# Optimization experiments

Hardware: AMD Instinct MI355X
Metric: run time of the kernel (lower is better)

The kernel has to match this reference:

```python
import jax, jax.numpy as jnp
import numpy as np

EPS = 1e-4
HEADS = 8
DIM_HEAD = 32
BALANCE = 0.3


def _normalize(x, dims):
    # torch normalize(): norm over `dims` in fp32; norm = eps + norm*sqrt(norm.numel()/x.numel())
    red = 1
    for d in dims:
        red *= x.shape[d]
    norm = jnp.sqrt(jnp.sum(jnp.square(x.astype(jnp.float32)), axis=dims, keepdims=True))
    norm = EPS + norm / np.sqrt(red)
    return x / norm.astype(x.dtype)


def _mpconv1x1(x, w, gain=1.0):
    # MPConv forward (eval mode): weight-normalize per output channel, scale, 1x1 conv
    w = w.astype(jnp.float32)
    w = _normalize(w, (1, 2, 3))
    fan_in = w.shape[1] * w.shape[2] * w.shape[3]
    w = (w * (gain / np.sqrt(fan_in))).astype(x.dtype)[:, :, 0, 0]  # [out, in]
    return jnp.einsum('oi,nihw->nohw', w, x)


def setup_inputs() -> dict:
    key = jax.random.key(0)
    k1, k2, k3 = jax.random.split(key, 3)
    x = jax.random.normal(k1, (2, 256, 48, 48), dtype=jnp.float32)
    w_qkv = jax.random.normal(k2, (768, 256, 1, 1), dtype=jnp.float32)
    w_out = jax.random.normal(k3, (256, 256, 1, 1), dtype=jnp.float32)
    return {"x": x, "w_qkv": w_qkv, "w_out": w_out}


def reference(x, w_qkv, w_out):
    n, c, h, w_sp = x.shape
    seq = h * w_sp
    y = _mpconv1x1(x, w_qkv)                          # [n, 3c, h, w]
    y = y.reshape(n, HEADS, DIM_HEAD, 3, seq)         # channel split: head x dim_head x 3
    y = _normalize(y, (2,))                           # L2-normalize over dim_head axis
    q = y[:, :, :, 0, :]
    k = y[:, :, :, 1, :]
    v = y[:, :, :, 2, :]
    # scores [n, h, q, k] with k scaled by 1/sqrt(dim_head)
    att = jax.nn.softmax(jnp.einsum('nhcq,nhck->nhqk', q, k) / np.sqrt(DIM_HEAD), axis=3)
    y = jnp.einsum('nhqk,nhck->nhcq', att, v)         # [n, heads, dim_head, seq]
    y = _mpconv1x1(y.reshape(n, c, h, w_sp), w_out)
    t = BALANCE
    # mp_sum: lerp then magnitude-preserving rescale
    return (x + t * (y - x)) / np.sqrt((1 - t) ** 2 + t ** 2)
```

## Files before the change

### kernel.cpp

```cpp
#include <hip/hip_runtime.h>
#include <math.h>

#define EPSN 1e-4f
#define SEQ 2304

using bf16x8 = __attribute__((ext_vector_type(8))) short;
using f32x4  = __attribute__((ext_vector_type(4))) float;

__device__ inline unsigned short f2bf(float x) {
    union { float f; unsigned u; } c; c.f = x;
    unsigned u = c.u;
    u += 0x7fffu + ((u >> 16) & 1u);
    return (unsigned short)(u >> 16);
}
__device__ inline float bf2f(unsigned short b) {
    union { unsigned u; float f; } c; c.u = ((unsigned)b) << 16;
    return c.f;
}

__global__ __launch_bounds__(256) void wnorm_kernel(const float* __restrict__ w_qkv,
                                                    const float* __restrict__ w_out,
                                                    unsigned short* __restrict__ wqb,
                                                    unsigned short* __restrict__ wob) {
    int row = blockIdx.x;
    const float* src;
    unsigned short* dst;
    if (row < 768) { src = w_qkv + row * 256; dst = wqb + row * 256; }
    else           { src = w_out + (row - 768) * 256; dst = wob + (row - 768) * 256; }
    float v = src[threadIdx.x];
    float ss = v * v;
    for (int off = 32; off > 0; off >>= 1) ss += __shfl_down(ss, off, 64);
    __shared__ float red[4];
    __shared__ float scale_s;
    int lane = threadIdx.x & 63, wid = threadIdx.x >> 6;
    if (lane == 0) red[wid] = ss;
    __syncthreads();
    if (threadIdx.x == 0) {
        float t = red[0] + red[1] + red[2] + red[3];
        scale_s = 1.0f / (sqrtf(t) + 16.0f * EPSN);
    }
    __syncthreads();
    dst[threadIdx.x] = f2bf(v * scale_s);
}

__global__ __launch_bounds__(256) void xt_kernel(const float* __restrict__ x,
                                                 unsigned short* __restrict__ xt) {
    __shared__ __align__(16) unsigned short T[64][80];
    int st = blockIdx.x;
    int ct = blockIdx.y;
    int n  = blockIdx.z;
    int t = threadIdx.x;
#pragma unroll
    for (int p = 0; p < 4; ++p) {
        int e = t + p * 256;
        int c = e >> 4, sv = (e & 15) * 4;
        float4 v = *(const float4*)&x[(size_t)(n * 256 + ct * 64 + c) * SEQ + st * 64 + sv];
        T[sv + 0][c] = f2bf(v.x);
        T[sv + 1][c] = f2bf(v.y);
        T[sv + 2][c] = f2bf(v.z);
        T[sv + 3][c] = f2bf(v.w);
    }
    __syncthreads();
#pragma unroll
    for (int p = 0; p < 2; ++p) {
        int e = t + p * 256;
        int s = e >> 3, cb = (e & 7) * 8;
        uint4 v = *(const uint4*)&T[s][cb];
        *(uint4*)&xt[(size_t)(n * SEQ + st * 64 + s) * 256 + ct * 64 + cb] = v;
    }
}

__global__ __launch_bounds__(256) void qkv_gemm_kernel(const unsigned short* __restrict__ xt,
                                                       const unsigned short* __restrict__ wqb,
                                                       unsigned short* __restrict__ qkvb) {
    int mt = blockIdx.x;
    int st = blockIdx.y;
    int n  = blockIdx.z;
    int tid = threadIdx.x;
    int wave = tid >> 6, lane = tid & 63;
    int ln = lane & 15, quad = lane >> 4;
    int m0 = mt * 64 + wave * 16;
    const unsigned short* Abase = wqb + (size_t)(m0 + ln) * 256 + quad * 8;
    const unsigned short* Bbase = xt + (size_t)(n * SEQ + st * 64 + ln) * 256 + quad * 8;
    f32x4 acc[4] = {{0.f,0.f,0.f,0.f},{0.f,0.f,0.f,0.f},{0.f,0.f,0.f,0.f},{0.f,0.f,0.f,0.f}};
#pragma unroll
    for (int kc = 0; kc < 8; ++kc) {
        bf16x8 a = *(const bf16x8*)(Abase + kc * 32);
#pragma unroll
        for (int c = 0; c < 4; ++c) {
            bf16x8 b = *(const bf16x8*)(Bbase + (size_t)(c * 16) * 256 + kc * 32);
            acc[c] = __builtin_amdgcn_mfma_f32_16x16x32_bf16(a, b, acc[c], 0, 0, 0);
        }
    }
#pragma unroll
    for (int c = 0; c < 4; ++c)
#pragma unroll
        for (int r = 0; r < 4; ++r) {
            int o = m0 + quad * 4 + r;
            int h = o / 96, rr = o % 96;
            int d = rr / 3, wh = rr % 3;
            int s = st * 64 + c * 16 + ln;
            qkvb[((size_t)((n * 8 + h) * 3 + wh) * 32 + d) * SEQ + s] = f2bf(acc[c][r]);
        }
}

__global__ __launch_bounds__(256) void dnorm_bf16_kernel(const unsigned short* __restrict__ qkvb,
                                                         unsigned short* __restrict__ qn,
                                                         unsigned short* __restrict__ kn,
                                                         unsigned short* __restrict__ vn) {
    int nh = blockIdx.x;
    int s = blockIdx.y * 256 + threadIdx.x;
    const float qscale = 0.17677669529663687f;
#pragma unroll
    for (int which = 0; which < 3; ++which) {
        const unsigned short* base = qkvb + ((size_t)(nh * 3 + which) * 32) * SEQ + s;
        float v[32];
        float ss = 0.f;
#pragma unroll
        for (int d = 0; d < 32; ++d) { v[d] = bf2f(base[(size_t)d * SEQ]); ss += v[d] * v[d]; }
        float inv = 1.0f / (EPSN + sqrtf(ss * (1.0f / 32.0f)));
        if (which == 0) inv *= qscale;
        if (which == 2) {
            unsigned short* dst = vn + (size_t)nh * 73728 + s;
#pragma unroll
            for (int d = 0; d < 32; ++d) dst[(size_t)d * SEQ] = f2bf(v[d] * inv);
        } else {
            unsigned short* dst = (which ? kn : qn) + (size_t)nh * 73728 + (size_t)s * 32;
            unsigned wbuf[16];
#pragma unroll
            for (int j = 0; j < 16; ++j)
                wbuf[j] = (unsigned)f2bf(v[2 * j] * inv) | ((unsigned)f2bf(v[2 * j + 1] * inv) << 16);
#pragma unroll
            for (int j = 0; j < 4; ++j) {
                uint4 t = make_uint4(wbuf[4 * j], wbuf[4 * j + 1], wbuf[4 * j + 2], wbuf[4 * j + 3]);
                *(uint4*)(dst + j * 8) = t;
            }
        }
    }
}

__global__ __launch_bounds__(256) void attn_mfma_kernel(const unsigned short* __restrict__ qn,
                                                        const unsigned short* __restrict__ kn,
                                                        const unsigned short* __restrict__ vn,
                                                        float* __restrict__ Opart,
                                                        float* __restrict__ Lpart) {
    __shared__ __align__(16) unsigned short Ks[64][40];
    __shared__ __align__(16) unsigned short Vs[32][72];
    __shared__ __align__(16) unsigned short Ps[4][16][72];
    int tid = threadIdx.x;
    int wave = tid >> 6, lane = tid & 63;
    int ln = lane & 15, quad = lane >> 4;
    int qt = blockIdx.x, nh = blockIdx.y, kz = blockIdx.z;
    const unsigned short* Qg = qn + (size_t)nh * 73728;
    const unsigned short* Kg = kn + (size_t)nh * 73728;
    const unsigned short* Vg = vn + (size_t)nh * 73728;

    bf16x8 qf = *(const bf16x8*)(Qg + (size_t)(qt * 64 + wave * 16 + ln) * 32 + quad * 8);
    bf16x8 ones;
#pragma unroll
    for (int i = 0; i < 8; ++i) ones[i] = (short)0x3F80;

    f32x4 o0 = {0.f, 0.f, 0.f, 0.f};
    f32x4 o1 = {0.f, 0.f, 0.f, 0.f};
    f32x4 lac = {0.f, 0.f, 0.f, 0.f};

    for (int kt = kz * 18; kt < kz * 18 + 18; ++kt) {
        int k0 = kt * 64;
        __syncthreads();
        {
            uint4 t = *(const uint4*)(Kg + (size_t)k0 * 32 + tid * 8);
            *(uint4*)(&Ks[tid >> 2][(tid & 3) * 8]) = t;
        }
        {
            uint4 t = *(const uint4*)(Vg + (size_t)(tid >> 3) * SEQ + k0 + (tid & 7) * 8);
            *(uint4*)(&Vs[tid >> 3][(tid & 7) * 8]) = t;
        }
        __syncthreads();

        const f32x4 zero = {0.f, 0.f, 0.f, 0.f};
#pragma unroll
        for (int c = 0; c < 4; ++c) {
            bf16x8 kf = *(const bf16x8*)(&Ks[c * 16 + ln][quad * 8]);
            f32x4 sc = __builtin_amdgcn_mfma_f32_16x16x32_bf16(qf, kf, zero, 0, 0, 0);
#pragma unroll
            for (int r = 0; r < 4; ++r)
                Ps[wave][quad * 4 + r][c * 16 + ln] = f2bf(__expf(sc[r]));
        }
        __syncthreads();

#pragma unroll
        for (int kc = 0; kc < 2; ++kc) {
            bf16x8 pf = *(const bf16x8*)(&Ps[wave][ln][kc * 32 + quad * 8]);
            bf16x8 v0 = *(const bf16x8*)(&Vs[ln][kc * 32 + quad * 8]);
            bf16x8 v1 = *(const bf16x8*)(&Vs[16 + ln][kc * 32 + quad * 8]);
            lac = __builtin_amdgcn_mfma_f32_16x16x32_bf16(pf, ones, lac, 0, 0, 0);
            o0  = __builtin_amdgcn_mfma_f32_16x16x32_bf16(pf, v0, o0, 0, 0, 0);
            o1  = __builtin_amdgcn_mfma_f32_16x16x32_bf16(pf, v1, o1, 0, 0, 0);
        }
    }

    float* Ob = Opart + ((size_t)(kz * 16 + nh) * 36 + qt) * 2048;
    float* Lb = Lpart + ((size_t)(kz * 16 + nh) * 36 + qt) * 64;
#pragma unroll
    for (int r = 0; r < 4; ++r) {
        int ql = wave * 16 + quad * 4 + r;
        Ob[ql * 32 + ln]      = o0[r];
        Ob[ql * 32 + 16 + ln] = o1[r];
        if (ln == 0) Lb[ql] = lac[r];
    }
}

__global__ __launch_bounds__(256) void attn_reduce_kernel(const float* __restrict__ Opart,
                                                          const float* __restrict__ Lpart,
                                                          unsigned short* __restrict__ y2t) {
    int qt = blockIdx.x, nh = blockIdx.y;
    int n = nh >> 3, h = nh & 7;
    const float* O0 = Opart + ((size_t)nh * 36 + qt) * 2048;
    const float* O1 = Opart + ((size_t)(16 + nh) * 36 + qt) * 2048;
    const float* L0 = Lpart + ((size_t)nh * 36 + qt) * 64;
    const float* L1 = Lpart + ((size_t)(16 + nh) * 36 + qt) * 64;
#pragma unroll
    for (int p = 0; p < 8; ++p) {
        int idx = threadIdx.x + p * 256;
        int q = idx >> 5, c = idx & 31;
        float l = L0[q] + L1[q];
        float v = (O0[idx] + O1[idx]) / l;
        y2t[((size_t)(n * SEQ) + qt * 64 + q) * 256 + h * 32 + c] = f2bf(v);
    }
}

__global__ __launch_bounds__(256) void out_gemm_kernel(const unsigned short* __restrict__ y2t,
                                                       const unsigned short* __restrict__ wob,
                                                       const float* __restrict__ x,
                                                       float* __restrict__ out) {
    int mt = blockIdx.x;
    int st = blockIdx.y;
    int n  = blockIdx.z;
    int tid = threadIdx.x;
    int wave = tid >> 6, lane = tid & 63;
    int ln = lane & 15, quad = lane >> 4;
    int m0 = mt * 64 + wave * 16;
    const unsigned short* Abase = wob + (size_t)(m0 + ln) * 256 + quad * 8;
    const unsigned short* Bbase = y2t + (size_t)(n * SEQ + st * 64 + ln) * 256 + quad * 8;
    f32x4 acc[4] = {{0.f,0.f,0.f,0.f},{0.f,0.f,0.f,0.f},{0.f,0.f,0.f,0.f},{0.f,0.f,0.f,0.f}};
#pragma unroll
    for (int kc = 0; kc < 8; ++kc) {
        bf16x8 a = *(const bf16x8*)(Abase + kc * 32);
#pragma unroll
        for (int c = 0; c < 4; ++c) {
            bf16x8 b = *(const bf16x8*)(Bbase + (size_t)(c * 16) * 256 + kc * 32);
            acc[c] = __builtin_amdgcn_mfma_f32_16x16x32_bf16(a, b, acc[c], 0, 0, 0);
        }
    }
    const float c0f = 0.7f * 1.3130643285972254f;
    const float c1f = 0.3f * 1.3130643285972254f;
#pragma unroll
    for (int c = 0; c < 4; ++c)
#pragma unroll
        for (int r = 0; r < 4; ++r) {
            int o = m0 + quad * 4 + r;
            int s = st * 64 + c * 16 + ln;
            size_t idx = (size_t)(n * 256 + o) * SEQ + s;
            out[idx] = c0f * x[idx] + c1f * acc[c][r];
        }
}

extern "C" void kernel_launch(void* const* d_in, const int* in_sizes, int n_in,
                              void* d_out, int out_size, void* d_ws, size_t ws_size,
                              hipStream_t stream) {
    (void)in_sizes; (void)n_in; (void)out_size; (void)ws_size;
    const float* x     = (const float*)d_in[0];
    const float* w_qkv = (const float*)d_in[1];
    const float* w_out = (const float*)d_in[2];
    float* out = (float*)d_out;
    float* ws  = (float*)d_ws;
    unsigned short* xt   = (unsigned short*)(ws);
    unsigned short* wqb  = (unsigned short*)(ws + 589824);
    unsigned short* qkvb = (unsigned short*)(ws + 688128);
    float* Opart = ws;
    float* Lpart = ws + 2359296;
    unsigned short* wob = (unsigned short*)(ws + 2457600);
    unsigned short* qn  = (unsigned short*)(ws + 2490368);
    unsigned short* kn  = (unsigned short*)(ws + 3080192);
    unsigned short* vn  = (unsigned short*)(ws + 3670016);
    unsigned short* y2t = (unsigned short*)(ws + 4259840);

    hipLaunchKernelGGL(wnorm_kernel, dim3(1024), dim3(256), 0, stream,
                       w_qkv, w_out, wqb, wob);
    hipLaunchKernelGGL(xt_kernel, dim3(36, 4, 2), dim3(256), 0, stream, x, xt);
    hipLaunchKernelGGL(qkv_gemm_kernel, dim3(12, 36, 2), dim3(256), 0, stream,
                       xt, wqb, qkvb);
    hipLaunchKernelGGL(dnorm_bf16_kernel, dim3(16, 9), dim3(256), 0, stream,
                       qkvb, qn, kn, vn);
    hipLaunchKernelGGL(attn_mfma_kernel, dim3(36, 16, 2), dim3(256), 0, stream,
                       qn, kn, vn, Opart, Lpart);
    hipLaunchKernelGGL(attn_reduce_kernel, dim3(36, 16), dim3(256), 0, stream,
                       Opart, Lpart, y2t);
    hipLaunchKernelGGL(out_gemm_kernel, dim3(4, 36, 2), dim3(256), 0, stream,
                       y2t, wob, x, out);
}
```

Measured before the change: 144.0 us.

## Fuse qkv GEMM with head norm, double-buffer attention, fuse reduce into out GEMM

```diff
diff --git a/kernel.cpp b/kernel.cpp
--- a/kernel.cpp
+++ b/kernel.cpp
@@ -12,10 +12,6 @@
     unsigned u = c.u;
     u += 0x7fffu + ((u >> 16) & 1u);
     return (unsigned short)(u >> 16);
-}
-__device__ inline float bf2f(unsigned short b) {
-    union { unsigned u; float f; } c; c.u = ((unsigned)b) << 16;
-    return c.f;
 }
 
 __global__ __launch_bounds__(256) void wnorm_kernel(const float* __restrict__ w_qkv,
@@ -70,70 +66,62 @@
     }
 }
 
-__global__ __launch_bounds__(256) void qkv_gemm_kernel(const unsigned short* __restrict__ xt,
-                                                       const unsigned short* __restrict__ wqb,
-                                                       unsigned short* __restrict__ qkvb) {
-    int mt = blockIdx.x;
+__global__ __launch_bounds__(256) void qkv_fused_kernel(const unsigned short* __restrict__ xt,
+                                                        const unsigned short* __restrict__ wqb,
+                                                        unsigned short* __restrict__ qn,
+                                                        unsigned short* __restrict__ kn,
+                                                        unsigned short* __restrict__ vn) {
+    __shared__ float Cs[96][65];
+    int h  = blockIdx.x;
     int st = blockIdx.y;
     int n  = blockIdx.z;
     int tid = threadIdx.x;
     int wave = tid >> 6, lane = tid & 63;
     int ln = lane & 15, quad = lane >> 4;
-    int m0 = mt * 64 + wave * 16;
-    const unsigned short* Abase = wqb + (size_t)(m0 + ln) * 256 + quad * 8;
-    const unsigned short* Bbase = xt + (size_t)(n * SEQ + st * 64 + ln) * 256 + quad * 8;
-    f32x4 acc[4] = {{0.f,0.f,0.f,0.f},{0.f,0.f,0.f,0.f},{0.f,0.f,0.f,0.f},{0.f,0.f,0.f,0.f}};
+    const unsigned short* Abase = wqb + (size_t)(h * 96 + ln) * 256 + quad * 8;
+    const unsigned short* Bbase = xt + (size_t)(n * SEQ + st * 64 + wave * 16 + ln) * 256 + quad * 8;
+    f32x4 acc[6];
+#pragma unroll
+    for (int m = 0; m < 6; ++m) acc[m] = (f32x4){0.f, 0.f, 0.f, 0.f};
 #pragma unroll
     for (int kc = 0; kc < 8; ++kc) {
-        bf16x8 a = *(const bf16x8*)(Abase + kc * 32);
-#pragma unroll
-        for (int c = 0; c < 4; ++c) {
-            bf16x8 b = *(const bf16x8*)(Bbase + (size_t)(c * 16) * 256 + kc * 32);
-            acc[c] = __builtin_amdgcn_mfma_f32_16x16x32_bf16(a, b, acc[c], 0, 0, 0);
-        }
-    }
-#pragma unroll
-    for (int c = 0; c < 4; ++c)
-#pragma unroll
-        for (int r = 0; r < 4; ++r) {
-            int o = m0 + quad * 4 + r;
-            int h = o / 96, rr = o % 96;
-            int d = rr / 3, wh = rr % 3;
-            int s = st * 64 + c * 16 + ln;
-            qkvb[((size_t)((n * 8 + h) * 3 + wh) * 32 + d) * SEQ + s] = f2bf(acc[c][r]);
-        }
-}
-
-__global__ __launch_bounds__(256) void dnorm_bf16_kernel(const unsigned short* __restrict__ qkvb,
-                                                         unsigned short* __restrict__ qn,
-                                                         unsigned short* __restrict__ kn,
-                                                         unsigned short* __restrict__ vn) {
-    int nh = blockIdx.x;
-    int s = blockIdx.y * 256 + threadIdx.x;
-    const float qscale = 0.17677669529663687f;
-#pragma unroll
-    for (int which = 0; which < 3; ++which) {
-        const unsigned short* base = qkvb + ((size_t)(nh * 3 + which) * 32) * SEQ + s;
+        bf16x8 b = *(const bf16x8*)(Bbase + kc * 32);
+#pragma unroll
+        for (int m = 0; m < 6; ++m) {
+            bf16x8 a = *(const bf16x8*)(Abase + (size_t)(m * 16) * 256 + kc * 32);
+            acc[m] = __builtin_amdgcn_mfma_f32_16x16x32_bf16(a, b, acc[m], 0, 0, 0);
+        }
+    }
+#pragma unroll
+    for (int m = 0; m < 6; ++m)
+#pragma unroll
+        for (int r = 0; r < 4; ++r)
+            Cs[m * 16 + quad * 4 + r][wave * 16 + ln] = acc[m][r];
+    __syncthreads();
+    if (tid < 192) {
+        int sl = tid & 63, wh = tid >> 6;
+        int s = st * 64 + sl;
+        int nh = n * 8 + h;
         float v[32];
         float ss = 0.f;
 #pragma unroll
-        for (int d = 0; d < 32; ++d) { v[d] = bf2f(base[(size_t)d * SEQ]); ss += v[d] * v[d]; }
+        for (int d = 0; d < 32; ++d) { v[d] = Cs[3 * d + wh][sl]; ss += v[d] * v[d]; }
         float inv = 1.0f / (EPSN + sqrtf(ss * (1.0f / 32.0f)));
-        if (which == 0) inv *= qscale;
-        if (which == 2) {
+        if (wh == 0) inv *= 0.17677669529663687f;
+        if (wh == 2) {
             unsigned short* dst = vn + (size_t)nh * 73728 + s;
 #pragma unroll
             for (int d = 0; d < 32; ++d) dst[(size_t)d * SEQ] = f2bf(v[d] * inv);
         } else {
-            unsigned short* dst = (which ? kn : qn) + (size_t)nh * 73728 + (size_t)s * 32;
+            unsigned short* dst = (wh == 1 ? kn : qn) + (size_t)nh * 73728 + (size_t)s * 32;
             unsigned wbuf[16];
 #pragma unroll
             for (int j = 0; j < 16; ++j)
                 wbuf[j] = (unsigned)f2bf(v[2 * j] * inv) | ((unsigned)f2bf(v[2 * j + 1] * inv) << 16);
 #pragma unroll
             for (int j = 0; j < 4; ++j) {
-                uint4 t = make_uint4(wbuf[4 * j], wbuf[4 * j + 1], wbuf[4 * j + 2], wbuf[4 * j + 3]);
-                *(uint4*)(dst + j * 8) = t;
+                uint4 t4 = make_uint4(wbuf[4 * j], wbuf[4 * j + 1], wbuf[4 * j + 2], wbuf[4 * j + 3]);
+                *(uint4*)(dst + j * 8) = t4;
             }
         }
     }
@@ -144,8 +132,8 @@
                                                         const unsigned short* __restrict__ vn,
                                                         float* __restrict__ Opart,
                                                         float* __restrict__ Lpart) {
-    __shared__ __align__(16) unsigned short Ks[64][40];
-    __shared__ __align__(16) unsigned short Vs[32][72];
+    __shared__ __align__(16) unsigned short Ks[2][64][40];
+    __shared__ __align__(16) unsigned short Vs[2][32][72];
     __shared__ __align__(16) unsigned short Ps[4][16][72];
     int tid = threadIdx.x;
     int wave = tid >> 6, lane = tid & 63;
@@ -164,38 +152,42 @@
     f32x4 o1 = {0.f, 0.f, 0.f, 0.f};
     f32x4 lac = {0.f, 0.f, 0.f, 0.f};
 
-    for (int kt = kz * 18; kt < kz * 18 + 18; ++kt) {
-        int k0 = kt * 64;
+    int kt0 = kz * 12;
+    uint4 kreg = *(const uint4*)(Kg + (size_t)(kt0 * 64) * 32 + tid * 8);
+    uint4 vreg = *(const uint4*)(Vg + (size_t)(tid >> 3) * SEQ + kt0 * 64 + (tid & 7) * 8);
+    *(uint4*)(&Ks[0][tid >> 2][(tid & 3) * 8]) = kreg;
+    *(uint4*)(&Vs[0][tid >> 3][(tid & 7) * 8]) = vreg;
+
+    for (int i = 0; i < 12; ++i) {
+        int buf = i & 1;
+        if (i + 1 < 12) {
+            int k0n = (kt0 + i + 1) * 64;
+            kreg = *(const uint4*)(Kg + (size_t)k0n * 32 + tid * 8);
+            vreg = *(const uint4*)(Vg + (size_t)(tid >> 3) * SEQ + k0n + (tid & 7) * 8);
+        }
         __syncthreads();
-        {
-            uint4 t = *(const uint4*)(Kg + (size_t)k0 * 32 + tid * 8);
-            *(uint4*)(&Ks[tid >> 2][(tid & 3) * 8]) = t;
-        }
-        {
-            uint4 t = *(const uint4*)(Vg + (size_t)(tid >> 3) * SEQ + k0 + (tid & 7) * 8);
-            *(uint4*)(&Vs[tid >> 3][(tid & 7) * 8]) = t;
-        }
-        __syncthreads();
 
         const f32x4 zero = {0.f, 0.f, 0.f, 0.f};
 #pragma unroll
         for (int c = 0; c < 4; ++c) {
-            bf16x8 kf = *(const bf16x8*)(&Ks[c * 16 + ln][quad * 8]);
+            bf16x8 kf = *(const bf16x8*)(&Ks[buf][c * 16 + ln][quad * 8]);
             f32x4 sc = __builtin_amdgcn_mfma_f32_16x16x32_bf16(qf, kf, zero, 0, 0, 0);
 #pragma unroll
             for (int r = 0; r < 4; ++r)
                 Ps[wave][quad * 4 + r][c * 16 + ln] = f2bf(__expf(sc[r]));
         }
-        __syncthreads();
-
 #pragma unroll
         for (int kc = 0; kc < 2; ++kc) {
             bf16x8 pf = *(const bf16x8*)(&Ps[wave][ln][kc * 32 + quad * 8]);
-            bf16x8 v0 = *(const bf16x8*)(&Vs[ln][kc * 32 + quad * 8]);
-            bf16x8 v1 = *(const bf16x8*)(&Vs[16 + ln][kc * 32 + quad * 8]);
+            bf16x8 v0 = *(const bf16x8*)(&Vs[buf][ln][kc * 32 + quad * 8]);
+            bf16x8 v1 = *(const bf16x8*)(&Vs[buf][16 + ln][kc * 32 + quad * 8]);
             lac = __builtin_amdgcn_mfma_f32_16x16x32_bf16(pf, ones, lac, 0, 0, 0);
             o0  = __builtin_amdgcn_mfma_f32_16x16x32_bf16(pf, v0, o0, 0, 0, 0);
             o1  = __builtin_amdgcn_mfma_f32_16x16x32_bf16(pf, v1, o1, 0, 0, 0);
+        }
+        if (i + 1 < 12) {
+            *(uint4*)(&Ks[buf ^ 1][tid >> 2][(tid & 3) * 8]) = kreg;
+            *(uint4*)(&Vs[buf ^ 1][tid >> 3][(tid & 7) * 8]) = vreg;
         }
     }
 
@@ -210,29 +202,11 @@
     }
 }
 
-__global__ __launch_bounds__(256) void attn_reduce_kernel(const float* __restrict__ Opart,
-                                                          const float* __restrict__ Lpart,
-                                                          unsigned short* __restrict__ y2t) {
-    int qt = blockIdx.x, nh = blockIdx.y;
-    int n = nh >> 3, h = nh & 7;
-    const float* O0 = Opart + ((size_t)nh * 36 + qt) * 2048;
-    const float* O1 = Opart + ((size_t)(16 + nh) * 36 + qt) * 2048;
-    const float* L0 = Lpart + ((size_t)nh * 36 + qt) * 64;
-    const float* L1 = Lpart + ((size_t)(16 + nh) * 36 + qt) * 64;
-#pragma unroll
-    for (int p = 0; p < 8; ++p) {
-        int idx = threadIdx.x + p * 256;
-        int q = idx >> 5, c = idx & 31;
-        float l = L0[q] + L1[q];
-        float v = (O0[idx] + O1[idx]) / l;
-        y2t[((size_t)(n * SEQ) + qt * 64 + q) * 256 + h * 32 + c] = f2bf(v);
-    }
-}
-
-__global__ __launch_bounds__(256) void out_gemm_kernel(const unsigned short* __restrict__ y2t,
-                                                       const unsigned short* __restrict__ wob,
-                                                       const float* __restrict__ x,
-                                                       float* __restrict__ out) {
+__global__ __launch_bounds__(256) void out_fused_kernel(const float* __restrict__ Opart,
+                                                        const float* __restrict__ Lpart,
+                                                        const unsigned short* __restrict__ wob,
+                                                        const float* __restrict__ x,
+                                                        float* __restrict__ out) {
     int mt = blockIdx.x;
     int st = blockIdx.y;
     int n  = blockIdx.z;
@@ -241,14 +215,32 @@
     int ln = lane & 15, quad = lane >> 4;
     int m0 = mt * 64 + wave * 16;
     const unsigned short* Abase = wob + (size_t)(m0 + ln) * 256 + quad * 8;
-    const unsigned short* Bbase = y2t + (size_t)(n * SEQ + st * 64 + ln) * 256 + quad * 8;
-    f32x4 acc[4] = {{0.f,0.f,0.f,0.f},{0.f,0.f,0.f,0.f},{0.f,0.f,0.f,0.f},{0.f,0.f,0.f,0.f}};
+    f32x4 acc[4];
+#pragma unroll
+    for (int c = 0; c < 4; ++c) acc[c] = (f32x4){0.f, 0.f, 0.f, 0.f};
 #pragma unroll
     for (int kc = 0; kc < 8; ++kc) {
+        int nh = n * 8 + kc;
         bf16x8 a = *(const bf16x8*)(Abase + kc * 32);
 #pragma unroll
         for (int c = 0; c < 4; ++c) {
-            bf16x8 b = *(const bf16x8*)(Bbase + (size_t)(c * 16) * 256 + kc * 32);
+            int q = c * 16 + ln;
+            float s0[8] = {0.f, 0.f, 0.f, 0.f, 0.f, 0.f, 0.f, 0.f};
+            float l = 0.f;
+#pragma unroll
+            for (int kzi = 0; kzi < 3; ++kzi) {
+                size_t slot = (size_t)(kzi * 16 + nh) * 36 + st;
+                const float* Ob = Opart + slot * 2048 + q * 32 + quad * 8;
+                float4 a0 = *(const float4*)Ob;
+                float4 a1 = *(const float4*)(Ob + 4);
+                s0[0] += a0.x; s0[1] += a0.y; s0[2] += a0.z; s0[3] += a0.w;
+                s0[4] += a1.x; s0[5] += a1.y; s0[6] += a1.z; s0[7] += a1.w;
+                l += Lpart[slot * 64 + q];
+            }
+            float inv = 1.0f / l;
+            bf16x8 b;
+#pragma unroll
+            for (int j = 0; j < 8; ++j) b[j] = (short)f2bf(s0[j] * inv);
             acc[c] = __builtin_amdgcn_mfma_f32_16x16x32_bf16(a, b, acc[c], 0, 0, 0);
         }
     }
@@ -274,28 +266,22 @@
     const float* w_out = (const float*)d_in[2];
     float* out = (float*)d_out;
     float* ws  = (float*)d_ws;
-    unsigned short* xt   = (unsigned short*)(ws);
-    unsigned short* wqb  = (unsigned short*)(ws + 589824);
-    unsigned short* qkvb = (unsigned short*)(ws + 688128);
-    float* Opart = ws;
-    float* Lpart = ws + 2359296;
-    unsigned short* wob = (unsigned short*)(ws + 2457600);
-    unsigned short* qn  = (unsigned short*)(ws + 2490368);
-    unsigned short* kn  = (unsigned short*)(ws + 3080192);
-    unsigned short* vn  = (unsigned short*)(ws + 3670016);
-    unsigned short* y2t = (unsigned short*)(ws + 4259840);
+    unsigned short* wqb = (unsigned short*)(ws);
+    unsigned short* wob = (unsigned short*)(ws + 98304);
+    unsigned short* xt  = (unsigned short*)(ws + 131072);
+    unsigned short* qn  = (unsigned short*)(ws + 720896);
+    unsigned short* kn  = (unsigned short*)(ws + 1310720);
+    unsigned short* vn  = (unsigned short*)(ws + 1900544);
+    float* Opart = ws + 2490368;
+    float* Lpart = ws + 6029312;
 
     hipLaunchKernelGGL(wnorm_kernel, dim3(1024), dim3(256), 0, stream,
                        w_qkv, w_out, wqb, wob);
     hipLaunchKernelGGL(xt_kernel, dim3(36, 4, 2), dim3(256), 0, stream, x, xt);
-    hipLaunchKernelGGL(qkv_gemm_kernel, dim3(12, 36, 2), dim3(256), 0, stream,
-                       xt, wqb, qkvb);
-    hipLaunchKernelGGL(dnorm_bf16_kernel, dim3(16, 9), dim3(256), 0, stream,
-                       qkvb, qn, kn, vn);
-    hipLaunchKernelGGL(attn_mfma_kernel, dim3(36, 16, 2), dim3(256), 0, stream,
+    hipLaunchKernelGGL(qkv_fused_kernel, dim3(8, 36, 2), dim3(256), 0, stream,
+                       xt, wqb, qn, kn, vn);
+    hipLaunchKernelGGL(attn_mfma_kernel, dim3(36, 16, 3), dim3(256), 0, stream,
                        qn, kn, vn, Opart, Lpart);
-    hipLaunchKernelGGL(attn_reduce_kernel, dim3(36, 16), dim3(256), 0, stream,
-                       Opart, Lpart, y2t);
-    hipLaunchKernelGGL(out_gemm_kernel, dim3(4, 36, 2), dim3(256), 0, stream,
-                       y2t, wob, x, out);
-}
+    hipLaunchKernelGGL(out_fused_kernel, dim3(4, 36, 2), dim3(256), 0, stream,
+                       Opart, Lpart, wob, x, out);
+}
```

After: 177.7 us. 23.4% more time.
